# Performance work log

Measured on AMD Instinct MI355X. Metric: run time of the kernel, lower is better.

Reference implementation:

```python
import jax, jax.numpy as jnp
import numpy as np

C = 256          # embed_dim
NH = 8           # n_heads
NL = 4           # n_levels
NP = 4           # n_points
HD = C // NH     # head dim = 32
SS = np.array([[128, 128], [64, 64], [32, 32], [16, 16]], dtype=np.int64)  # (H_l, W_l)
LSI = np.concatenate([[0], np.cumsum(SS[:, 0] * SS[:, 1])[:-1]]).astype(np.int64)
LIN = int((SS[:, 0] * SS[:, 1]).sum())  # 21760
B = 2
LQ = LIN


def setup_inputs() -> dict:
    key = jax.random.key(0)
    ks = jax.random.split(key, 8)
    s = 0.02
    return {
        "query": jax.random.normal(ks[0], (B, LQ, C), jnp.float32),
        "reference_points": jax.random.uniform(ks[1], (B, LQ, NL, 2), dtype=jnp.float32),
        "input_flatten": jax.random.normal(ks[2], (B, LIN, C), jnp.float32),
        "W_value": jax.random.normal(ks[3], (C, C), jnp.float32) * s,
        "b_value": jnp.zeros((C,), jnp.float32),
        "W_off": jax.random.normal(ks[4], (C, NH * NL * NP * 2), jnp.float32) * s,
        "b_off": jnp.zeros((NH * NL * NP * 2,), jnp.float32),
        "W_attn": jax.random.normal(ks[5], (C, NH * NL * NP), jnp.float32) * s,
        "b_attn": jnp.zeros((NH * NL * NP,), jnp.float32),
        "W_out": jax.random.normal(ks[6], (C, C), jnp.float32) * s,
        "b_out": jnp.zeros((C,), jnp.float32),
        "input_spatial_shapes": jnp.asarray(SS),
        "input_level_start_index": jnp.asarray(LSI),
    }


def _msda(query, reference_points, input_flatten,
          W_value, b_value, W_off, b_off, W_attn, b_attn, W_out, b_out):
    N, Lq, _ = query.shape
    Lin = input_flatten.shape[1]
    # projections
    value = (input_flatten @ W_value + b_value).reshape(N, Lin, NH, HD)
    off = (query @ W_off + b_off).reshape(N, Lq, NH, NL, NP, 2)
    aw = jax.nn.softmax((query @ W_attn + b_attn).reshape(N, Lq, NH, NL * NP), axis=-1)
    aw = aw.reshape(N, Lq, NH, NL, NP)
    # normalizer is (W_l, H_l) per level
    norm = jnp.asarray(SS[:, ::-1].copy(), jnp.float32)  # (NL, 2)
    loc = reference_points[:, :, None, :, None, :] + off / norm[None, None, None, :, None, :]
    out = jnp.zeros((N, Lq, NH, HD), query.dtype)
    for l in range(NL):
        Hl, Wl = int(SS[l, 0]), int(SS[l, 1])
        st = int(LSI[l])
        v = value[:, st:st + Hl * Wl].transpose(0, 2, 1, 3)  # (N, NH, HW, HD)
        # grid_sample align_corners=False semantics: pixel = loc*size - 0.5
        x = loc[:, :, :, l, :, 0] * Wl - 0.5  # (N, Lq, NH, NP)
        y = loc[:, :, :, l, :, 1] * Hl - 0.5
        x0 = jnp.floor(x)
        y0 = jnp.floor(y)
        lw = x - x0
        lh = y - y0
        x0i = x0.astype(jnp.int32)
        y0i = y0.astype(jnp.int32)

        def corner(ix, iy, w):
            valid = (ix >= 0) & (ix < Wl) & (iy >= 0) & (iy < Hl)
            idx = jnp.clip(iy * Wl + ix, 0, Hl * Wl - 1)
            idx_t = idx.transpose(0, 2, 1, 3).reshape(N, NH, Lq * NP)
            g = jnp.take_along_axis(v, idx_t[:, :, :, None], axis=2)
            g = g.reshape(N, NH, Lq, NP, HD)
            wt = (w * valid).transpose(0, 2, 1, 3)  # (N, NH, Lq, NP)
            return g * wt[..., None]

        samp = (corner(x0i, y0i, (1 - lw) * (1 - lh))
                + corner(x0i + 1, y0i, lw * (1 - lh))
                + corner(x0i, y0i + 1, (1 - lw) * lh)
                + corner(x0i + 1, y0i + 1, lw * lh))
        out = out + jnp.einsum('nhqpd,nqhp->nqhd', samp, aw[:, :, :, l])
    return out.reshape(N, Lq, C) @ W_out + b_out


def reference(query, reference_points, input_flatten,
              W_value, b_value, W_off, b_off, W_attn, b_attn, W_out, b_out,
              input_spatial_shapes, input_level_start_index):
    return _msda(query, reference_points, input_flatten,
                 W_value, b_value, W_off, b_off, W_attn, b_attn, W_out, b_out)
```

## Files before the change

### kernel.cpp

```cpp
#include <hip/hip_runtime.h>

typedef unsigned short u16;
typedef unsigned int u32;
typedef short bf16x8 __attribute__((ext_vector_type(8)));
typedef float f32x4 __attribute__((ext_vector_type(4)));

#define LQ_ 21760
#define LIN_ 21760
#define CDIM 256
#define MROWS (2 * LQ_)

__device__ __forceinline__ u16 f2bf(float f) {
  u32 u;
  __builtin_memcpy(&u, &f, 4);
  u32 r = (u + 0x7fffu + ((u >> 16) & 1u)) >> 16;
  return (u16)r;
}
__device__ __forceinline__ u32 pack_bf16_rne(float a, float b) {
  return (u32)f2bf(a) | ((u32)f2bf(b) << 16);
}
__device__ __forceinline__ float bflo(u32 u) {
  u32 v = u << 16;
  float f;
  __builtin_memcpy(&f, &v, 4);
  return f;
}
__device__ __forceinline__ float bfhi(u32 u) {
  u32 v = u & 0xffff0000u;
  float f;
  __builtin_memcpy(&f, &v, 4);
  return f;
}

__device__ __forceinline__ void conv_one(const float* W0, const float* W1, u16* Wf,
                                         int N, int split, int blk, int t) {
  const int tid = blk * 256 + t;
  if (tid >= N * 32) return;
  const int n = tid >> 5, kcg = tid & 31;
  float w[8];
#pragma unroll
  for (int j = 0; j < 8; ++j) {
    const int k = kcg * 8 + j;
    w[j] = (n < split) ? W0[(size_t)k * split + n]
                       : W1[(size_t)k * (N - split) + (n - split)];
  }
  uint4 pk;
  pk.x = pack_bf16_rne(w[0], w[1]);
  pk.y = pack_bf16_rne(w[2], w[3]);
  pk.z = pack_bf16_rne(w[4], w[5]);
  pk.w = pack_bf16_rne(w[6], w[7]);
  const int ks = kcg >> 2, kcr = kcg & 3, c = n >> 4;
  const int chunk = ks * (N / 4) + c * 4 + kcr;
  *(uint4*)(Wf + (size_t)chunk * 128 + (n & 15) * 8) = pk;
}

__global__ __launch_bounds__(256) void conv_fused(
    const float* __restrict__ Wv, const float* __restrict__ Wof,
    const float* __restrict__ Wa, const float* __restrict__ Wo,
    const float* __restrict__ bof, const float* __restrict__ ba,
    u16* __restrict__ WfV, u16* __restrict__ WfC, u16* __restrict__ WfO,
    float* __restrict__ bcat, const float* __restrict__ Aq,
    const float* __restrict__ Ai, u16* __restrict__ Qf, u16* __restrict__ If) {
  const int b = blockIdx.x, t = threadIdx.x;
  if (b < 32) {
    conv_one(Wv, Wv, WfV, 256, 256, b, t);
    return;
  }
  if (b < 80) {
    conv_one(Wof, Wa, WfC, 384, 256, b - 32, t);
    return;
  }
  if (b < 112) {
    conv_one(Wo, Wo, WfO, 256, 256, b - 80, t);
    return;
  }
  if (b < 114) {
    const int i = (b - 112) * 256 + t;
    if (i < 384) bcat[i] = (i < 256) ? bof[i] : ba[i - 256];
    return;
  }
  const int i = (b - 114) * 256 + t;
  const int n4 = MROWS * 32;
  const float* src;
  u16* dst;
  int j;
  if (i < n4) {
    src = Aq;
    dst = Qf;
    j = i;
  } else {
    src = Ai;
    dst = If;
    j = i - n4;
  }
  const int tile = j >> 9;
  const int c2 = (j >> 4) & 31;
  const int sr = j & 15;
  const int row = (tile >> 3) * 128 + (c2 >> 2) * 16 + sr;
  const int kc = (tile & 7) * 32 + (c2 & 3) * 8;
  const float4 f0 = *(const float4*)(src + (size_t)row * 256 + kc);
  const float4 f1 = *(const float4*)(src + (size_t)row * 256 + kc + 4);
  uint4 pk;
  pk.x = pack_bf16_rne(f0.x, f0.y);
  pk.y = pack_bf16_rne(f0.z, f0.w);
  pk.z = pack_bf16_rne(f1.x, f1.y);
  pk.w = pack_bf16_rne(f1.z, f1.w);
  *(uint4*)(dst + (size_t)j * 8) = pk;
}

__global__ __launch_bounds__(256) void gemm_vq(
    const u16* __restrict__ If, const u16* __restrict__ WfV,
    const float* __restrict__ bv, u16* __restrict__ outV,
    const u16* __restrict__ Qf, const u16* __restrict__ WfC,
    const float* __restrict__ bcat, float* __restrict__ outO,
    float* __restrict__ outA) {
  const int t = threadIdx.x, l = t & 63, wv = t >> 6;
  const int wr = wv >> 1, wc = wv & 1;
  const int fq = l >> 4, fr = l & 15;
  bf16x8 af[8][4];

  if (blockIdx.x < 340) {
    const int rb = blockIdx.x;
    const u16* ab = If + (size_t)rb * 32768 + (wr * 16 + fq) * 128 + fr * 8;
#pragma unroll
    for (int ks = 0; ks < 8; ++ks)
#pragma unroll
      for (int r = 0; r < 4; ++r)
        af[ks][r] = *(const bf16x8*)(ab + ks * 4096 + r * 512);
#pragma unroll
    for (int cb = 0; cb < 2; ++cb) {
      f32x4 acc[4][4];
#pragma unroll
      for (int r = 0; r < 4; ++r)
#pragma unroll
        for (int c = 0; c < 4; ++c) acc[r][c] = f32x4{0.f, 0.f, 0.f, 0.f};
      const u16* bb = WfV + ((size_t)(cb * 8 + wc * 4) * 4 + fq) * 128 + fr * 8;
#pragma unroll
      for (int ks = 0; ks < 8; ++ks) {
        bf16x8 bf[4];
#pragma unroll
        for (int c = 0; c < 4; ++c) bf[c] = *(const bf16x8*)(bb + ks * 8192 + c * 512);
#pragma unroll
        for (int c = 0; c < 4; ++c)
#pragma unroll
          for (int r = 0; r < 4; ++r)
            acc[r][c] = __builtin_amdgcn_mfma_f32_16x16x32_bf16(af[ks][r], bf[c],
                                                                acc[r][c], 0, 0, 0);
      }
      const int rq = fq * 4;
#pragma unroll
      for (int c = 0; c < 4; ++c) {
        const int col = cb * 128 + wc * 64 + c * 16 + fr;
        const float bz = bv[col];
#pragma unroll
        for (int r = 0; r < 4; ++r) {
          const int row0 = rb * 128 + wr * 64 + r * 16 + rq;
#pragma unroll
          for (int g = 0; g < 4; ++g)
            outV[(size_t)(row0 + g) * 256 + col] = f2bf(acc[r][c][g] + bz);
        }
      }
    }
  } else {
    const int rb = blockIdx.x - 340;
    const u16* ab = Qf + (size_t)rb * 32768 + (wr * 16 + fq) * 128 + fr * 8;
#pragma unroll
    for (int ks = 0; ks < 8; ++ks)
#pragma unroll
      for (int r = 0; r < 4; ++r)
        af[ks][r] = *(const bf16x8*)(ab + ks * 4096 + r * 512);
#pragma unroll
    for (int cb = 0; cb < 3; ++cb) {
      f32x4 acc[4][4];
#pragma unroll
      for (int r = 0; r < 4; ++r)
#pragma unroll
        for (int c = 0; c < 4; ++c) acc[r][c] = f32x4{0.f, 0.f, 0.f, 0.f};
      const u16* bb = WfC + ((size_t)(cb * 8 + wc * 4) * 4 + fq) * 128 + fr * 8;
#pragma unroll
      for (int ks = 0; ks < 8; ++ks) {
        bf16x8 bf[4];
#pragma unroll
        for (int c = 0; c < 4; ++c) bf[c] = *(const bf16x8*)(bb + ks * 12288 + c * 512);
#pragma unroll
        for (int c = 0; c < 4; ++c)
#pragma unroll
          for (int r = 0; r < 4; ++r)
            acc[r][c] = __builtin_amdgcn_mfma_f32_16x16x32_bf16(af[ks][r], bf[c],
                                                                acc[r][c], 0, 0, 0);
      }
      const int rq = fq * 4;
#pragma unroll
      for (int c = 0; c < 4; ++c) {
        const int col = cb * 128 + wc * 64 + c * 16 + fr;
        const float bz = bcat[col];
#pragma unroll
        for (int r = 0; r < 4; ++r) {
          const int row0 = rb * 128 + wr * 64 + r * 16 + rq;
#pragma unroll
          for (int g = 0; g < 4; ++g) {
            const float v = acc[r][c][g] + bz;
            if (col < 256)
              outO[(size_t)(row0 + g) * 256 + col] = v;
            else
              outA[(size_t)(row0 + g) * 128 + (col - 256)] = v;
          }
        }
      }
    }
  }
}

__global__ __launch_bounds__(256) void gemm_out(
    const u16* __restrict__ A, const u16* __restrict__ Wf,
    const float* __restrict__ bias, float* __restrict__ out) {
  const int rb = blockIdx.x;
  const int t = threadIdx.x, l = t & 63, wv = t >> 6;
  const int wr = wv >> 1, wc = wv & 1;
  const int fq = l >> 4, fr = l & 15;
  bf16x8 af[8][4];
  const u16* ab = A + ((size_t)rb * 128 + wr * 64 + fr) * 256 + fq * 8;
#pragma unroll
  for (int ks = 0; ks < 8; ++ks)
#pragma unroll
    for (int r = 0; r < 4; ++r)
      af[ks][r] = *(const bf16x8*)(ab + (size_t)r * 4096 + ks * 32);
#pragma unroll
  for (int cb = 0; cb < 2; ++cb) {
    f32x4 acc[4][4];
#pragma unroll
    for (int r = 0; r < 4; ++r)
#pragma unroll
      for (int c = 0; c < 4; ++c) acc[r][c] = f32x4{0.f, 0.f, 0.f, 0.f};
    const u16* bb = Wf + ((size_t)(cb * 8 + wc * 4) * 4 + fq) * 128 + fr * 8;
#pragma unroll
    for (int ks = 0; ks < 8; ++ks) {
      bf16x8 bf[4];
#pragma unroll
      for (int c = 0; c < 4; ++c) bf[c] = *(const bf16x8*)(bb + ks * 8192 + c * 512);
#pragma unroll
      for (int c = 0; c < 4; ++c)
#pragma unroll
        for (int r = 0; r < 4; ++r)
          acc[r][c] = __builtin_amdgcn_mfma_f32_16x16x32_bf16(af[ks][r], bf[c],
                                                              acc[r][c], 0, 0, 0);
    }
    const int rq = fq * 4;
#pragma unroll
    for (int c = 0; c < 4; ++c) {
      const int col = cb * 128 + wc * 64 + c * 16 + fr;
      const float bz = bias[col];
#pragma unroll
      for (int r = 0; r < 4; ++r) {
        const int row0 = rb * 128 + wr * 64 + r * 16 + rq;
#pragma unroll
        for (int g = 0; g < 4; ++g)
          out[(size_t)(row0 + g) * 256 + col] = acc[r][c][g] + bz;
      }
    }
  }
}

__global__ __launch_bounds__(256) void msda_sample3(
    const u16* __restrict__ value, const float* __restrict__ off,
    const float* __restrict__ attnl, const float* __restrict__ refp,
    u16* __restrict__ out) {
  __shared__ float s_aw[64 * 17];
  __shared__ uint4 s_idx[16 * 64];
  __shared__ float4 s_w[16 * 64];
  const int t = threadIdx.x;
  const int bq0 = blockIdx.x * 8;

  if (t < 64) {
    const float* lg = attnl + (size_t)(bq0 + (t >> 3)) * 128 + (t & 7) * 16;
    float e[16];
    float m = -1e30f;
#pragma unroll
    for (int i = 0; i < 16; ++i) {
      e[i] = lg[i];
      m = fmaxf(m, e[i]);
    }
    float s = 0.f;
#pragma unroll
    for (int i = 0; i < 16; ++i) {
      e[i] = __expf(e[i] - m);
      s += e[i];
    }
    const float inv = 1.f / s;
#pragma unroll
    for (int i = 0; i < 16; ++i) s_aw[t * 17 + i] = e[i] * inv;
  }
  __syncthreads();

#pragma unroll
  for (int rr = 0; rr < 4; ++rr) {
    const int id = t + rr * 256;
    const int qh = id & 63, lp = id >> 6;
    const int q = qh >> 3, h = qh & 7, lv = lp >> 2, p = lp & 3;
    const int bq = bq0 + q;
    const int Wl = 128 >> lv;
    const int st = (lv == 0) ? 0 : (lv == 1) ? 16384 : (lv == 2) ? 20480 : 21504;
    const float ox = off[(size_t)bq * 256 + ((h * 4 + lv) * 4 + p) * 2];
    const float oy = off[(size_t)bq * 256 + ((h * 4 + lv) * 4 + p) * 2 + 1];
    const float rx = refp[(size_t)bq * 8 + lv * 2];
    const float ry = refp[(size_t)bq * 8 + lv * 2 + 1];
    const float aw = s_aw[qh * 17 + lp];
    const float x = rx * (float)Wl + ox - 0.5f;
    const float y = ry * (float)Wl + oy - 0.5f;
    const float xf = floorf(x), yf = floorf(y);
    const int x0 = (int)xf, y0 = (int)yf;
    const float lw = x - xf, lh = y - yf;
    const float hw = 1.f - lw, hh = 1.f - lh;
    const int ixs[4] = {x0, x0 + 1, x0, x0 + 1};
    const int iys[4] = {y0, y0, y0 + 1, y0 + 1};
    const float wts[4] = {hw * hh, lw * hh, hw * lh, lw * lh};
    u32 rows[4];
    float ws4[4];
#pragma unroll
    for (int c = 0; c < 4; ++c) {
      const int ix = ixs[c], iy = iys[c];
      const bool valid = (ix >= 0) & (ix < Wl) & (iy >= 0) & (iy < Wl);
      int idx = iy * Wl + ix;
      idx = max(0, min(idx, Wl * Wl - 1));
      rows[c] = (u32)(st + idx);
      ws4[c] = valid ? (wts[c] * aw) : 0.f;
    }
    uint4 iv;
    iv.x = rows[0];
    iv.y = rows[1];
    iv.z = rows[2];
    iv.w = rows[3];
    s_idx[lp * 64 + qh] = iv;
    s_w[lp * 64 + qh] = make_float4(ws4[0], ws4[1], ws4[2], ws4[3]);
  }
  __syncthreads();

  const int q = t >> 5, h = (t >> 2) & 7, dg = t & 3;
  const int qh = q * 8 + h;
  const int bq = bq0 + q;
  const u16* vp = value + (size_t)((bq >= LQ_) ? LIN_ : 0) * CDIM + h * 32 + dg * 8;
  float a0 = 0.f, a1 = 0.f, a2 = 0.f, a3 = 0.f;
  float a4 = 0.f, a5 = 0.f, a6 = 0.f, a7 = 0.f;
#pragma unroll 4
  for (int lp = 0; lp < 16; ++lp) {
    const uint4 iv = s_idx[lp * 64 + qh];
    const float4 wv = s_w[lp * 64 + qh];
    const u32 rows[4] = {iv.x, iv.y, iv.z, iv.w};
    const float ww[4] = {wv.x, wv.y, wv.z, wv.w};
#pragma unroll
    for (int c = 0; c < 4; ++c) {
      const uint4 d = *(const uint4*)(vp + (size_t)rows[c] * CDIM);
      const float w = ww[c];
      a0 += w * bflo(d.x);
      a1 += w * bfhi(d.x);
      a2 += w * bflo(d.y);
      a3 += w * bfhi(d.y);
      a4 += w * bflo(d.z);
      a5 += w * bfhi(d.z);
      a6 += w * bflo(d.w);
      a7 += w * bfhi(d.w);
    }
  }
  uint4 o;
  o.x = pack_bf16_rne(a0, a1);
  o.y = pack_bf16_rne(a2, a3);
  o.z = pack_bf16_rne(a4, a5);
  o.w = pack_bf16_rne(a6, a7);
  *(uint4*)(out + (size_t)bq * CDIM + h * 32 + dg * 8) = o;
}

extern "C" void kernel_launch(void* const* d_in, const int* in_sizes, int n_in,
                              void* d_out, int out_size, void* d_ws, size_t ws_size,
                              hipStream_t stream) {
  const float* query = (const float*)d_in[0];
  const float* refp = (const float*)d_in[1];
  const float* inflat = (const float*)d_in[2];
  const float* Wv = (const float*)d_in[3];
  const float* bv = (const float*)d_in[4];
  const float* Wof = (const float*)d_in[5];
  const float* bof = (const float*)d_in[6];
  const float* Wa = (const float*)d_in[7];
  const float* ba = (const float*)d_in[8];
  const float* Wo = (const float*)d_in[9];
  const float* bo = (const float*)d_in[10];
  float* out = (float*)d_out;

  const size_t M = MROWS;

  u16* If = (u16*)d_ws;
  u16* Qf = If + M * 256;
  u16* ws_value = Qf + M * 256;
  float* ws_off = (float*)(ws_value + M * 256);
  float* ws_attn = ws_off + M * 256;
  u16* WfV = (u16*)(ws_attn + M * 128);
  u16* WfC = WfV + 256 * 256;
  u16* WfO = WfC + 384 * 256;
  float* bcat = (float*)(WfO + 256 * 256);
  u16* ws_samp = If;

  conv_fused<<<dim3(10994), dim3(256), 0, stream>>>(Wv, Wof, Wa, Wo, bof, ba, WfV, WfC,
                                                    WfO, bcat, query, inflat, Qf, If);
  gemm_vq<<<dim3(680), dim3(256), 0, stream>>>(If, WfV, bv, ws_value, Qf, WfC, bcat,
                                               ws_off, ws_attn);
  msda_sample3<<<dim3(5440), dim3(256), 0, stream>>>(ws_value, ws_off, ws_attn, refp,
                                                     ws_samp);
  gemm_out<<<dim3(340), dim3(256), 0, stream>>>(ws_samp, WfO, bo, out);
}
```

Baseline: 287.7 us.

## Store value projection in per-level head-major row layout for sampling locality

```diff
diff --git a/kernel.cpp b/kernel.cpp
--- a/kernel.cpp
+++ b/kernel.cpp
@@ -9,6 +9,7 @@
 #define LIN_ 21760
 #define CDIM 256
 #define MROWS (2 * LQ_)
+#define VUNITS 174080
 
 __device__ __forceinline__ u16 f2bf(float f) {
   u32 u;
@@ -127,6 +128,21 @@
 #pragma unroll
       for (int r = 0; r < 4; ++r)
         af[ks][r] = *(const bf16x8*)(ab + ks * 4096 + r * 512);
+    const int b = (rb >= 170);
+    const int rb0 = rb - b * 170;
+    int ubase, sstart, logW;
+    if (rb0 < 128) {
+      ubase = 0; sstart = 0; logW = 7;
+    } else if (rb0 < 160) {
+      ubase = 131072; sstart = 16384; logW = 6;
+    } else if (rb0 < 168) {
+      ubase = 163840; sstart = 20480; logW = 5;
+    } else {
+      ubase = 172032; sstart = 21504; logW = 4;
+    }
+    const int Wm1 = (1 << logW) - 1;
+    const int ubb = b * VUNITS + ubase;
+    const int srow = rb * 128 - b * 21760 - sstart;
 #pragma unroll
     for (int cb = 0; cb < 2; ++cb) {
       f32x4 acc[4][4];
@@ -151,13 +167,18 @@
 #pragma unroll
       for (int c = 0; c < 4; ++c) {
         const int col = cb * 128 + wc * 64 + c * 16 + fr;
+        const int h = col >> 5, d = col & 31;
         const float bz = bv[col];
 #pragma unroll
         for (int r = 0; r < 4; ++r) {
-          const int row0 = rb * 128 + wr * 64 + r * 16 + rq;
-#pragma unroll
-          for (int g = 0; g < 4; ++g)
-            outV[(size_t)(row0 + g) * 256 + col] = f2bf(acc[r][c][g] + bz);
+          const int s0 = srow + wr * 64 + r * 16 + rq;
+#pragma unroll
+          for (int g = 0; g < 4; ++g) {
+            const int s = s0 + g;
+            const int y = s >> logW, x = s & Wm1;
+            const int unit = ubb + (((y << 3) + h) << logW) + x;
+            outV[(size_t)unit * 32 + d] = f2bf(acc[r][c][g] + bz);
+          }
         }
       }
     }
@@ -298,8 +319,9 @@
     const int qh = id & 63, lp = id >> 6;
     const int q = qh >> 3, h = qh & 7, lv = lp >> 2, p = lp & 3;
     const int bq = bq0 + q;
-    const int Wl = 128 >> lv;
-    const int st = (lv == 0) ? 0 : (lv == 1) ? 16384 : (lv == 2) ? 20480 : 21504;
+    const int logW = 7 - lv;
+    const int Wl = 1 << logW;
+    const int ub = (lv == 0) ? 0 : (lv == 1) ? 131072 : (lv == 2) ? 163840 : 172032;
     const float ox = off[(size_t)bq * 256 + ((h * 4 + lv) * 4 + p) * 2];
     const float oy = off[(size_t)bq * 256 + ((h * 4 + lv) * 4 + p) * 2 + 1];
     const float rx = refp[(size_t)bq * 8 + lv * 2];
@@ -311,34 +333,32 @@
     const int x0 = (int)xf, y0 = (int)yf;
     const float lw = x - xf, lh = y - yf;
     const float hw = 1.f - lw, hh = 1.f - lh;
-    const int ixs[4] = {x0, x0 + 1, x0, x0 + 1};
-    const int iys[4] = {y0, y0, y0 + 1, y0 + 1};
-    const float wts[4] = {hw * hh, lw * hh, hw * lh, lw * lh};
-    u32 rows[4];
-    float ws4[4];
-#pragma unroll
-    for (int c = 0; c < 4; ++c) {
-      const int ix = ixs[c], iy = iys[c];
-      const bool valid = (ix >= 0) & (ix < Wl) & (iy >= 0) & (iy < Wl);
-      int idx = iy * Wl + ix;
-      idx = max(0, min(idx, Wl * Wl - 1));
-      rows[c] = (u32)(st + idx);
-      ws4[c] = valid ? (wts[c] * aw) : 0.f;
-    }
+    const int x0c = min(max(x0, 0), Wl - 1);
+    const int x1c = min(max(x0 + 1, 0), Wl - 1);
+    const int y0c = min(max(y0, 0), Wl - 1);
+    const int y1c = min(max(y0 + 1, 0), Wl - 1);
+    const bool vx0 = (x0 >= 0) & (x0 < Wl);
+    const bool vx1 = (x0 + 1 >= 0) & (x0 + 1 < Wl);
+    const bool vy0 = (y0 >= 0) & (y0 < Wl);
+    const bool vy1 = (y0 + 1 >= 0) & (y0 + 1 < Wl);
+    const int base0 = ub + (((y0c << 3) + h) << logW);
+    const int base1 = ub + (((y1c << 3) + h) << logW);
     uint4 iv;
-    iv.x = rows[0];
-    iv.y = rows[1];
-    iv.z = rows[2];
-    iv.w = rows[3];
+    iv.x = (u32)(base0 + x0c);
+    iv.y = (u32)(base0 + x1c);
+    iv.z = (u32)(base1 + x0c);
+    iv.w = (u32)(base1 + x1c);
     s_idx[lp * 64 + qh] = iv;
-    s_w[lp * 64 + qh] = make_float4(ws4[0], ws4[1], ws4[2], ws4[3]);
+    s_w[lp * 64 + qh] =
+        make_float4((vx0 & vy0) ? hw * hh * aw : 0.f, (vx1 & vy0) ? lw * hh * aw : 0.f,
+                    (vx0 & vy1) ? hw * lh * aw : 0.f, (vx1 & vy1) ? lw * lh * aw : 0.f);
   }
   __syncthreads();
 
   const int q = t >> 5, h = (t >> 2) & 7, dg = t & 3;
   const int qh = q * 8 + h;
   const int bq = bq0 + q;
-  const u16* vp = value + (size_t)((bq >= LQ_) ? LIN_ : 0) * CDIM + h * 32 + dg * 8;
+  const u16* vp = value + (size_t)((bq >= LQ_) ? VUNITS : 0) * 32 + dg * 8;
   float a0 = 0.f, a1 = 0.f, a2 = 0.f, a3 = 0.f;
   float a4 = 0.f, a5 = 0.f, a6 = 0.f, a7 = 0.f;
 #pragma unroll 4
@@ -349,7 +369,7 @@
     const float ww[4] = {wv.x, wv.y, wv.z, wv.w};
 #pragma unroll
     for (int c = 0; c < 4; ++c) {
-      const uint4 d = *(const uint4*)(vp + (size_t)rows[c] * CDIM);
+      const uint4 d = *(const uint4*)(vp + (size_t)rows[c] * 32);
       const float w = ww[c];
       a0 += w * bflo(d.x);
       a1 += w * bfhi(d.x);
```

New measurement: 295.1 us. 2.6% more time.
